# Kernel optimization log

Hardware: AMD Instinct MI355X
Metric: run time of the kernel (lower is better)

## Reference

```python
import jax, jax.numpy as jnp
import numpy as np

HIDDEN = 512

def setup_inputs() -> dict:
    key = jax.random.key(0)
    k1, k2 = jax.random.split(key)
    lstm_output = jax.random.normal(k1, (64, 4096, HIDDEN), dtype=jnp.float32)
    # nn.Linear(hidden,1,bias=False): weight [1,hidden]; store as [hidden] vector
    w_attn = jax.random.normal(k2, (HIDDEN,), dtype=jnp.float32) * (1.0 / np.sqrt(HIDDEN))
    return {"lstm_output": lstm_output, "w_attn": w_attn}

def reference(lstm_output, w_attn):
    # scores: [B,S] = lstm_output @ w
    scores = jnp.einsum('bsh,h->bs', lstm_output, w_attn)
    weights = jax.nn.softmax(scores, axis=1)            # [B,S]
    pooled = jnp.einsum('bs,bsh->bh', weights, lstm_output)  # [B,H]
    return (pooled, weights)
```

## Files before the change

### kernel.cpp

```cpp
#include <hip/hip_runtime.h>
#include <math.h>

#define B 64
#define S 4096
#define H 512
#define CH 32
#define SC (S / CH)

#define DOT8(xa, xc) ( (xa).x*wa.x + (xa).y*wa.y + (xa).z*wa.z + (xa).w*wa.w \
                     + (xc).x*wb.x + (xc).y*wb.y + (xc).z*wb.z + (xc).w*wb.w )
#define FMA4(acc, p, v) { (acc).x += (p)*(v).x; (acc).y += (p)*(v).y; \
                          (acc).z += (p)*(v).z; (acc).w += (p)*(v).w; }

__global__ __launch_bounds__(256) void attn_pass1(
    const float* __restrict__ x, const float* __restrict__ w,
    float* __restrict__ scores, float* __restrict__ pl,
    float* __restrict__ pacc)
{
    const int blk  = blockIdx.x;
    const int b    = blk >> 5;
    const int c    = blk & 31;
    const int tid  = threadIdx.x;
    const int wv   = tid >> 6;
    const int lane = tid & 63;

    const float4* w4 = (const float4*)w;
    const float4 wa = w4[lane];
    const float4 wb = w4[64 + lane];

    const float4* xb4 = (const float4*)(x + (size_t)b * S * H);
    const int s0 = c * SC;

    float  l0 = 0.f, l1 = 0.f;
    float4 a0a = make_float4(0.f,0.f,0.f,0.f), a0b = make_float4(0.f,0.f,0.f,0.f);
    float4 a1a = make_float4(0.f,0.f,0.f,0.f), a1b = make_float4(0.f,0.f,0.f,0.f);

    #pragma unroll 2
    for (int t = 0; t < 8; ++t) {
        const int i = 16 * t + 4 * wv;
        const float4* xp = xb4 + (size_t)(s0 + i) * (H / 4);
        const float4 xa0 = xp[lane],        xc0 = xp[ 64 + lane];
        const float4 xa1 = xp[128 + lane],  xc1 = xp[192 + lane];
        const float4 xa2 = xp[256 + lane],  xc2 = xp[320 + lane];
        const float4 xa3 = xp[384 + lane],  xc3 = xp[448 + lane];

        float d0 = DOT8(xa0, xc0);
        float d1 = DOT8(xa1, xc1);
        float d2 = DOT8(xa2, xc2);
        float d3 = DOT8(xa3, xc3);
        #pragma unroll
        for (int off = 32; off; off >>= 1) {
            d0 += __shfl_xor(d0, off);
            d1 += __shfl_xor(d1, off);
            d2 += __shfl_xor(d2, off);
            d3 += __shfl_xor(d3, off);
        }
        d0 = fminf(d0, 60.f); d1 = fminf(d1, 60.f);
        d2 = fminf(d2, 60.f); d3 = fminf(d3, 60.f);

        if (lane == 0)
            *(float4*)&scores[(size_t)b * S + s0 + i] = make_float4(d0, d1, d2, d3);

        const float p0 = __expf(d0), p1 = __expf(d1);
        const float p2 = __expf(d2), p3 = __expf(d3);
        l0 += p0 + p2; l1 += p1 + p3;
        FMA4(a0a, p0, xa0); FMA4(a0b, p0, xc0);
        FMA4(a1a, p1, xa1); FMA4(a1b, p1, xc1);
        FMA4(a0a, p2, xa2); FMA4(a0b, p2, xc2);
        FMA4(a1a, p3, xa3); FMA4(a1b, p3, xc3);
    }

    const float4 aa = make_float4(a0a.x+a1a.x, a0a.y+a1a.y, a0a.z+a1a.z, a0a.w+a1a.w);
    const float4 ab = make_float4(a0b.x+a1b.x, a0b.y+a1b.y, a0b.z+a1b.z, a0b.w+a1b.w);
    const float  lw = l0 + l1;

    __shared__ float sl[4];
    __shared__ float sacc[4][H];
    ((float4*)sacc[wv])[lane]      = aa;
    ((float4*)sacc[wv])[64 + lane] = ab;
    if (lane == 0) sl[wv] = lw;
    __syncthreads();

    const size_t pbase = (size_t)blk * H;
    pacc[pbase + tid]       = sacc[0][tid]     + sacc[1][tid]     + sacc[2][tid]     + sacc[3][tid];
    pacc[pbase + tid + 256] = sacc[0][tid+256] + sacc[1][tid+256] + sacc[2][tid+256] + sacc[3][tid+256];
    if (tid == 0) pl[blk] = sl[0] + sl[1] + sl[2] + sl[3];
}

__global__ __launch_bounds__(256) void attn_pass2(
    const float* __restrict__ pl, const float* __restrict__ pacc,
    float* __restrict__ pooled, float* __restrict__ bl)
{
    const int b   = blockIdx.x;
    const int tid = threadIdx.x;

    float L = 0.f, a0 = 0.f, a1 = 0.f;
    #pragma unroll
    for (int c = 0; c < CH; ++c) {
        L += pl[b * CH + c];
        const size_t base = (size_t)(b * CH + c) * H;
        a0 += pacc[base + tid];
        a1 += pacc[base + tid + 256];
    }
    const float inv = 1.f / L;
    pooled[(size_t)b * H + tid]       = a0 * inv;
    pooled[(size_t)b * H + tid + 256] = a1 * inv;
    if (tid == 0) bl[b] = inv;
}

__global__ __launch_bounds__(256) void attn_pass3(
    const float* __restrict__ scores, const float* __restrict__ bl,
    float* __restrict__ wout)
{
    const int i4 = blockIdx.x * 256 + threadIdx.x;
    const int b  = i4 >> 10;
    const float4 sc = ((const float4*)scores)[i4];
    const float inv = bl[b];
    float4 o;
    o.x = __expf(sc.x) * inv;
    o.y = __expf(sc.y) * inv;
    o.z = __expf(sc.z) * inv;
    o.w = __expf(sc.w) * inv;
    ((float4*)wout)[i4] = o;
}

extern "C" void kernel_launch(void* const* d_in, const int* in_sizes, int n_in,
                              void* d_out, int out_size, void* d_ws, size_t ws_size,
                              hipStream_t stream) {
    const float* x = (const float*)d_in[0];
    const float* w = (const float*)d_in[1];

    float* out     = (float*)d_out;
    float* pooled  = out;
    float* weights = out + (size_t)B * H;

    float* ws     = (float*)d_ws;
    float* scores = ws;
    float* pl     = scores + (size_t)B * S;
    float* pacc   = pl + B * CH;
    float* bl     = pacc + (size_t)B * CH * H;

    attn_pass1<<<B * CH, 256, 0, stream>>>(x, w, scores, pl, pacc);
    attn_pass2<<<B, 256, 0, stream>>>(pl, pacc, pooled, bl);
    attn_pass3<<<(B * S) / 4 / 256, 256, 0, stream>>>(scores, bl, weights);
}
```

Before: 674.8 us.

## Double-buffer pass1 input rows through LDS using direct global-to-LDS loads

After: 696.6 us. 1.03x slower.

```diff
diff --git a/kernel.cpp b/kernel.cpp
--- a/kernel.cpp
+++ b/kernel.cpp
@@ -6,11 +6,15 @@
 #define H 512
 #define CH 32
 #define SC (S / CH)
+#define TRIPS 16
 
 #define DOT8(xa, xc) ( (xa).x*wa.x + (xa).y*wa.y + (xa).z*wa.z + (xa).w*wa.w \
                      + (xc).x*wb.x + (xc).y*wb.y + (xc).z*wb.z + (xc).w*wb.w )
 #define FMA4(acc, p, v) { (acc).x += (p)*(v).x; (acc).y += (p)*(v).y; \
                           (acc).z += (p)*(v).z; (acc).w += (p)*(v).w; }
+
+typedef const __attribute__((address_space(1))) unsigned int* as1_u32p;
+typedef __attribute__((address_space(3))) unsigned int* as3_u32p;
 
 __global__ __launch_bounds__(256) void attn_pass1(
     const float* __restrict__ x, const float* __restrict__ w,
@@ -28,54 +32,67 @@
     const float4 wa = w4[lane];
     const float4 wb = w4[64 + lane];
 
-    const float4* xb4 = (const float4*)(x + (size_t)b * S * H);
     const int s0 = c * SC;
+    const float* xrow0 = x + (size_t)b * S * H + (size_t)s0 * H + lane * 4;
 
-    float  l0 = 0.f, l1 = 0.f;
+    __shared__ float buf[4][2][2][H];
+
+#define STAGE(t) { \
+    const float* g0 = xrow0 + (size_t)(8 * (t) + 2 * wv) * H; \
+    float* l = &buf[wv][(t) & 1][0][0]; \
+    __builtin_amdgcn_global_load_lds((as1_u32p)(g0),       (as3_u32p)(l),       16, 0, 0); \
+    __builtin_amdgcn_global_load_lds((as1_u32p)(g0 + 256), (as3_u32p)(l + 256), 16, 0, 0); \
+    __builtin_amdgcn_global_load_lds((as1_u32p)(g0 + 512), (as3_u32p)(l + 512), 16, 0, 0); \
+    __builtin_amdgcn_global_load_lds((as1_u32p)(g0 + 768), (as3_u32p)(l + 768), 16, 0, 0); \
+}
+
+    float  lsum0 = 0.f, lsum1 = 0.f;
     float4 a0a = make_float4(0.f,0.f,0.f,0.f), a0b = make_float4(0.f,0.f,0.f,0.f);
     float4 a1a = make_float4(0.f,0.f,0.f,0.f), a1b = make_float4(0.f,0.f,0.f,0.f);
 
-    #pragma unroll 2
-    for (int t = 0; t < 8; ++t) {
-        const int i = 16 * t + 4 * wv;
-        const float4* xp = xb4 + (size_t)(s0 + i) * (H / 4);
-        const float4 xa0 = xp[lane],        xc0 = xp[ 64 + lane];
-        const float4 xa1 = xp[128 + lane],  xc1 = xp[192 + lane];
-        const float4 xa2 = xp[256 + lane],  xc2 = xp[320 + lane];
-        const float4 xa3 = xp[384 + lane],  xc3 = xp[448 + lane];
+    STAGE(0)
+    #pragma unroll
+    for (int t = 0; t < TRIPS; ++t) {
+        if (t + 1 < TRIPS) {
+            STAGE(t + 1)
+            asm volatile("s_waitcnt vmcnt(4)" ::: "memory");
+        } else {
+            asm volatile("s_waitcnt vmcnt(0)" ::: "memory");
+        }
+        const float4* r0 = (const float4*)&buf[wv][t & 1][0][0];
+        const float4* r1 = (const float4*)&buf[wv][t & 1][1][0];
+        const float4 xa0 = r0[lane], xc0 = r0[64 + lane];
+        const float4 xa1 = r1[lane], xc1 = r1[64 + lane];
 
         float d0 = DOT8(xa0, xc0);
         float d1 = DOT8(xa1, xc1);
-        float d2 = DOT8(xa2, xc2);
-        float d3 = DOT8(xa3, xc3);
         #pragma unroll
         for (int off = 32; off; off >>= 1) {
             d0 += __shfl_xor(d0, off);
             d1 += __shfl_xor(d1, off);
-            d2 += __shfl_xor(d2, off);
-            d3 += __shfl_xor(d3, off);
         }
-        d0 = fminf(d0, 60.f); d1 = fminf(d1, 60.f);
-        d2 = fminf(d2, 60.f); d3 = fminf(d3, 60.f);
+        d0 = fminf(d0, 60.f);
+        d1 = fminf(d1, 60.f);
 
         if (lane == 0)
-            *(float4*)&scores[(size_t)b * S + s0 + i] = make_float4(d0, d1, d2, d3);
+            *(float2*)&scores[(size_t)b * S + s0 + 8 * t + 2 * wv] = make_float2(d0, d1);
 
         const float p0 = __expf(d0), p1 = __expf(d1);
-        const float p2 = __expf(d2), p3 = __expf(d3);
-        l0 += p0 + p2; l1 += p1 + p3;
+        lsum0 += p0; lsum1 += p1;
         FMA4(a0a, p0, xa0); FMA4(a0b, p0, xc0);
         FMA4(a1a, p1, xa1); FMA4(a1b, p1, xc1);
-        FMA4(a0a, p2, xa2); FMA4(a0b, p2, xc2);
-        FMA4(a1a, p3, xa3); FMA4(a1b, p3, xc3);
     }
+#undef STAGE
 
-    const float4 aa = make_float4(a0a.x+a1a.x, a0a.y+a1a.y, a0a.z+a1a.z, a0a.w+a1a.w);
-    const float4 ab = make_float4(a0b.x+a1b.x, a0b.y+a1b.y, a0b.z+a1b.z, a0b.w+a1b.w);
-    const float  lw = l0 + l1;
+    const float4 aa = make_float4(a0a.x + a1a.x, a0a.y + a1a.y,
+                                  a0a.z + a1a.z, a0a.w + a1a.w);
+    const float4 ab = make_float4(a0b.x + a1b.x, a0b.y + a1b.y,
+                                  a0b.z + a1b.z, a0b.w + a1b.w);
+    const float  lw = lsum0 + lsum1;
 
-    __shared__ float sl[4];
-    __shared__ float sacc[4][H];
+    __syncthreads();
+    float (*sacc)[H] = (float (*)[H])&buf[0][0][0][0];
+    float* sl        = &buf[1][0][0][0];
     ((float4*)sacc[wv])[lane]      = aa;
     ((float4*)sacc[wv])[64 + lane] = ab;
     if (lane == 0) sl[wv] = lw;
```
